# Kernel tuning notes

Hardware: AMD Instinct MI355X
Metric: run time of the kernel (lower is better)

Reference implementation:

```python
import jax, jax.numpy as jnp
import numpy as np

N_HEADS = 4

def _conv2d(x, w, b):
    # NCHW input, OIHW weight, 3x3 SAME, stride 1
    y = jax.lax.conv_general_dilated(x, w, window_strides=(1, 1), padding='SAME',
                                     dimension_numbers=('NCHW', 'OIHW', 'NCHW'))
    return y + b[None, :, None, None]


def setup_inputs() -> dict:
    key = jax.random.key(0)
    ks = jax.random.split(key, 5)
    x = jax.random.normal(ks[0], (4, 32, 256, 256), dtype=jnp.float32)
    conv1_w = jax.random.normal(ks[1], (384, 32, 3, 3), dtype=jnp.float32) * 0.05
    conv1_b = jax.random.normal(ks[2], (384,), dtype=jnp.float32) * 0.05
    conv2_w = jax.random.normal(ks[3], (32, 128, 3, 3), dtype=jnp.float32) * 0.05
    conv2_b = jax.random.normal(ks[4], (32,), dtype=jnp.float32) * 0.05
    return {'x': x, 'conv1_w': conv1_w, 'conv1_b': conv1_b,
            'conv2_w': conv2_w, 'conv2_b': conv2_b}


def reference(x, conv1_w, conv1_b, conv2_w, conv2_b):
    b, c_in, h, w = x.shape
    n = h * w
    qkv = _conv2d(x, conv1_w, conv1_b)              # [b, 3*heads*d, h, w]
    d = qkv.shape[1] // (3 * N_HEADS)               # head dim
    qkv = qkv.reshape(b, 3, N_HEADS, d, n)          # 'b (qkv heads c) h w -> b qkv heads c n'
    q, k, v = qkv[:, 0], qkv[:, 1], qkv[:, 2]
    k = jax.nn.softmax(k, axis=-1)                  # softmax over n = h*w
    weights = jnp.einsum('bhdn,bhen->bhde', q, k)   # [b, heads, d, d] context
    out = jnp.einsum('bhde,bhdn->bhen', weights, v) # [b, heads, d, n]
    out = out.reshape(b, N_HEADS * d, h, w)         # 'b heads c n -> b (heads c) h w'
    return _conv2d(out, conv2_w, conv2_b)
```

## Files before the change

kernel.cpp:

```cpp
#include <hip/hip_runtime.h>
#include <hip/hip_bf16.h>

typedef __hip_bfloat16 bf16;
typedef __attribute__((ext_vector_type(8))) short short8;
typedef __attribute__((ext_vector_type(4))) float f32x4;
typedef __attribute__((ext_vector_type(16))) float f32x16;

#define B_    4
#define CIN   32
#define HH    256
#define WW    256
#define C1    384
#define NPIX  65536
#define CMID  128
#define COUT  32
#define PW    258
#define VROW  16512

static __device__ __forceinline__ float u2f(unsigned short u) {
    unsigned int x = ((unsigned int)u) << 16;
    return __uint_as_float(x);
}
static __device__ __forceinline__ unsigned short f2u(float f) {
    bf16 h = __float2bfloat16(f);
    return __builtin_bit_cast(unsigned short, h);
}
static __device__ __forceinline__ unsigned int pk2(float lo, float hi) {
    return (unsigned int)f2u(lo) | ((unsigned int)f2u(hi) << 16);
}
static __device__ __forceinline__ void gload16(const void* src, void* dst) {
    __builtin_amdgcn_global_load_lds(
        (const __attribute__((address_space(1))) void*)src,
        (__attribute__((address_space(3))) void*)dst, 16, 0, 0);
}

__global__ __launch_bounds__(256) void k_w1t(const float* __restrict__ w1, short* __restrict__ w1t) {
    const int tap = blockIdx.x;
    for (int i = threadIdx.x; i < 384 * 32; i += 256) {
        int co = i >> 5, cij = i & 31;
        w1t[((size_t)(tap * 4 + (cij >> 3)) * 384 + co) * 8 + (cij & 7)] =
            (short)f2u(w1[(size_t)i * 9 + tap]);
    }
}

__global__ __launch_bounds__(256) void k_xt2(const float* __restrict__ x,
                                             unsigned short* __restrict__ xt2, int b0) {
    const int row = blockIdx.x, bl = blockIdx.y, b = b0 + bl;
    const int tx = threadIdx.x;
    unsigned short* rbase = xt2 + (size_t)(bl * PW + row) * 4 * PW * 8;
    const uint4 z = make_uint4(0u, 0u, 0u, 0u);
    if (row == 0 || row == PW - 1) {
        for (int i = tx; i < 4 * PW; i += 256) ((uint4*)rbase)[i] = z;
        return;
    }
    if (tx < 2) {
        int c = tx ? (PW - 1) : 0;
#pragma unroll
        for (int ch = 0; ch < 4; ch++)
            *(uint4*)(rbase + ((size_t)ch * PW + c) * 8) = z;
    }
    const int col = tx + 1;
    const size_t px = (size_t)(row - 1) * WW + tx;
    unsigned int pk[16];
#pragma unroll
    for (int c2 = 0; c2 < 16; c2++) {
        float v0 = x[((size_t)b * CIN + 2 * c2) * NPIX + px];
        float v1 = x[((size_t)b * CIN + 2 * c2 + 1) * NPIX + px];
        pk[c2] = pk2(v0, v1);
    }
#pragma unroll
    for (int ch = 0; ch < 4; ch++)
        *(uint4*)(rbase + ((size_t)ch * PW + col) * 8) =
            make_uint4(pk[ch * 4], pk[ch * 4 + 1], pk[ch * 4 + 2], pk[ch * 4 + 3]);
}

__global__ __launch_bounds__(256) void k_bordv(unsigned short* __restrict__ vt) {
    const int row = blockIdx.x, bp = blockIdx.y, tx = threadIdx.x;
    unsigned short* base = vt + ((size_t)bp * PW + row) * VROW;
    const uint4 z = make_uint4(0u, 0u, 0u, 0u);
    if (row == 0 || row == PW - 1) {
        for (int i = tx; i < VROW / 8; i += 256) ((uint4*)base)[i] = z;
    } else if (tx < 16) {
        int g = tx >> 1, c = (tx & 1) * (PW - 1);
        *(uint4*)(base + ((size_t)g * PW + c) * 8) = z;
    }
}

__global__ __launch_bounds__(256, 2) void k_conv1(
    const unsigned short* __restrict__ xt2, const short* __restrict__ w1t,
    const float* __restrict__ b1, unsigned short* __restrict__ vt,
    unsigned short* __restrict__ pw, float* __restrict__ ps, int nb)
{
    const int nblk = 512 * nb;
    const int m = ((int)blockIdx.x & 7) * (nblk >> 3) + ((int)blockIdx.x >> 3);
    const int chunk = m & 1;
    const int y   = (m >> 1) & 255;
    const int bl  = m >> 9;
    const int px0 = chunk * 128;
    const int cid = bl * 512 + y * 2 + chunk;
    const int tx  = threadIdx.x;
    const int wv  = tx >> 6, l = tx & 63;
    const int lhi = l >> 4, llo = l & 15;

    __shared__ short xs[12 * 132 * 8];
    union obuf {
        short os[64][136];
        short ost[128][66];
        short osw[4][32][32];
    };
    __shared__ obuf ou2[2];

#pragma unroll
    for (int i = 0; i < 3; i++) {
        int p = wv * 3 + i;
        int r = p >> 2, ch = p & 3;
        const char* src = (const char*)xt2 +
            (((size_t)(bl * PW) + y + r) * 4 + ch) * (PW * 16) + (size_t)px0 * 16 + (size_t)l * 16;
        char* dst = (char*)xs + p * 2112;
        gload16(src, dst);
        gload16(src + 1024, dst + 1024);
        if (l < 2) gload16(src + 2048, dst + 2048);
    }
    __syncthreads();

    const short* wbase = w1t + ((size_t)lhi * 384 + llo) * 8;

    short8 qa[2][4];
    f32x4 wacc[2][2];
#pragma unroll
    for (int dt = 0; dt < 2; dt++)
#pragma unroll
        for (int et = 0; et < 2; et++) wacc[dt][et] = (f32x4){0.f, 0.f, 0.f, 0.f};
    float se0 = 0.f, se1 = 0.f;

#pragma unroll
    for (int cog = 0; cog < 6; cog++) {
        const int co0 = cog * 64;
        const int p   = cog & 1;

        f32x4 acc[2][4];
#pragma unroll
        for (int t = 0; t < 2; t++)
#pragma unroll
            for (int mc = 0; mc < 4; mc++) acc[t][mc] = (f32x4){0.f, 0.f, 0.f, 0.f};

        short8 a[4], an[4];
#pragma unroll
        for (int mc = 0; mc < 4; mc++)
            an[mc] = *(const short8*)(wbase + ((size_t)co0 + mc * 16) * 8);
#pragma unroll
        for (int tap = 0; tap < 9; tap++) {
            const int dy = tap / 3, dx = tap % 3;
#pragma unroll
            for (int mc = 0; mc < 4; mc++) a[mc] = an[mc];
            if (tap < 8) {
#pragma unroll
                for (int mc = 0; mc < 4; mc++)
                    an[mc] = *(const short8*)(wbase +
                        ((size_t)(tap + 1) * 4 * 384 + co0 + mc * 16) * 8);
            }
#pragma unroll
            for (int t = 0; t < 2; t++) {
                short8 bfr = *(const short8*)&xs[(((dy * 4 + lhi) * 132) + (wv * 32 + t * 16 + llo + dx)) * 8];
#pragma unroll
                for (int mc = 0; mc < 4; mc++)
                    acc[t][mc] = __builtin_amdgcn_mfma_f32_16x16x32_bf16(a[mc], bfr, acc[t][mc], 0, 0, 0);
            }
        }

        float bias[4][4];
#pragma unroll
        for (int mc = 0; mc < 4; mc++)
#pragma unroll
            for (int r = 0; r < 4; r++)
                bias[mc][r] = b1[co0 + mc * 16 + lhi * 4 + r];

        if (cog < 4) {
#pragma unroll
            for (int t = 0; t < 2; t++)
#pragma unroll
                for (int mc = 0; mc < 4; mc++)
#pragma unroll
                    for (int r = 0; r < 4; r++)
                        ou2[p].os[mc * 16 + lhi * 4 + r][wv * 32 + t * 16 + llo] =
                            (short)f2u(acc[t][mc][r] + bias[mc][r]);
        } else {
#pragma unroll
            for (int t = 0; t < 2; t++)
#pragma unroll
                for (int mc = 0; mc < 4; mc++)
#pragma unroll
                    for (int r = 0; r < 4; r++)
                        ou2[p].ost[wv * 32 + t * 16 + llo][mc * 16 + lhi * 4 + r] =
                            (short)f2u(acc[t][mc][r] + bias[mc][r]);
        }
        __syncthreads();

        if (cog < 2) {
            if ((wv >> 1) == cog) {
                const int chb = (wv & 1) * 32;
#pragma unroll
                for (int dt = 0; dt < 2; dt++)
#pragma unroll
                    for (int ks = 0; ks < 4; ks++)
                        qa[dt][ks] = *(const short8*)&ou2[p].os[chb + dt * 16 + llo][ks * 32 + lhi * 8];
            }
        } else if (cog < 4) {
            if ((wv >> 1) == cog - 2) {
                const int chb = (wv & 1) * 32;
#pragma unroll
                for (int et = 0; et < 2; et++)
#pragma unroll
                    for (int ks = 0; ks < 4; ks++) {
                        short8 kf = *(const short8*)&ou2[p].os[chb + et * 16 + llo][ks * 32 + lhi * 8];
                        short8 pf;
#pragma unroll
                        for (int j = 0; j < 8; j++) {
                            float ef = __expf(u2f((unsigned short)kf[j]));
                            if (et == 0) se0 += ef; else se1 += ef;
                            pf[j] = (short)f2u(ef);
                        }
#pragma unroll
                        for (int dt = 0; dt < 2; dt++)
                            wacc[dt][et] = __builtin_amdgcn_mfma_f32_16x16x32_bf16(
                                qa[dt][ks], pf, wacc[dt][et], 0, 0, 0);
                    }
            }
        } else {
            const int plane = cog - 4;
            unsigned short* rowb = vt + ((size_t)(bl * 2 + plane) * PW + 1 + y) * VROW;
#pragma unroll
            for (int i = 0; i < 4; i++) {
                int u = i * 256 + tx;
                int g = u >> 7, px = u & 127;
                uint4 v = *(const uint4*)&ou2[p].ost[px][g * 8];
                *(uint4*)(rowb + ((size_t)g * PW + 1 + px0 + px) * 8) = v;
            }
        }
    }

    se0 += __shfl_xor(se0, 16); se0 += __shfl_xor(se0, 32);
    se1 += __shfl_xor(se1, 16); se1 += __shfl_xor(se1, 32);
    if (l < 16) {
        ps[(size_t)cid * 128 + wv * 32 + llo]      = se0;
        ps[(size_t)cid * 128 + wv * 32 + 16 + llo] = se1;
    }

#pragma unroll
    for (int dt = 0; dt < 2; dt++)
#pragma unroll
        for (int et = 0; et < 2; et++)
#pragma unroll
            for (int r = 0; r < 4; r++)
                ou2[0].osw[wv][dt * 16 + lhi * 4 + r][et * 16 + llo] = (short)f2u(wacc[dt][et][r]);
    __syncthreads();

    {
        unsigned short* pwp = pw + (size_t)cid * 4096;
        const unsigned short* osf = (const unsigned short*)&ou2[0];
#pragma unroll
        for (int p2 = 0; p2 < 2; p2++)
            *(uint4*)(pwp + p2 * 2048 + tx * 8) = *(const uint4*)(osf + p2 * 2048 + tx * 8);
    }
}

__global__ __launch_bounds__(256) void k_wred(
    const unsigned short* __restrict__ pw, const float* __restrict__ ps,
    float* __restrict__ wts, int b0)
{
    const int bh = blockIdx.x;
    const int jq = blockIdx.y;
    const int bl = bh >> 2, h = bh & 3;
    const int tx = threadIdx.x;
    __shared__ float rinvs[32];
    if (tx < 32) {
        float s = 0.f;
        const float* pp = ps + (size_t)bl * 512 * 128 + h * 32 + tx;
        for (int c = 0; c < 512; c++) s += pp[(size_t)c * 128];
        rinvs[tx] = 1.f / s;
    }
    __syncthreads();
    const int i = jq * 256 + tx;
    const unsigned short* pwp = pw + (size_t)bl * 512 * 4096 + h * 1024 + i;
    float s = 0.f;
    for (int c = 0; c < 512; c++) s += u2f(pwp[(size_t)c * 4096]);
    wts[(size_t)(b0 * 4 + bh) * 1024 + i] = s * rinvs[i & 31];
}

__global__ __launch_bounds__(256) void k_w2e(
    const float* __restrict__ w2, const float* __restrict__ wts,
    short* __restrict__ w2te, int b0)
{
    const int bl = blockIdx.x, tap = blockIdx.y;
    const int tx = threadIdx.x;
    __shared__ float Wsh[4096];
    __shared__ float w2sh[4096];
    for (int i = tx; i < 4096; i += 256) {
        Wsh[i]  = wts[(size_t)(b0 + bl) * 4096 + i];
        w2sh[i] = w2[(size_t)i * 9 + tap];
    }
    __syncthreads();
#pragma unroll
    for (int rep = 0; rep < 16; rep++) {
        int o = rep * 256 + tx;
        int cv = o >> 5, co = o & 31;
        int h = cv >> 5, d = cv & 31;
        const float* wp = &w2sh[co * 128 + 32 * h];
        const float* Wp = &Wsh[h * 1024 + d * 32];
        float s = 0.f;
#pragma unroll
        for (int e = 0; e < 32; e++) s += wp[e] * Wp[e];
        w2te[((((size_t)bl * 9 + tap) * 16 + (cv >> 3)) * 32 + co) * 8 + (cv & 7)] =
            (short)f2u(s);
    }
}

__global__ __launch_bounds__(256, 2) void k_conv2e(
    const unsigned short* __restrict__ vt, const short* __restrict__ w2te,
    const float* __restrict__ b2, float* __restrict__ out, int b0, int nb)
{
    const int nblk = 512 * nb;
    const int m = ((int)blockIdx.x & 7) * (nblk >> 3) + ((int)blockIdx.x >> 3);
    const int chunk = m & 1;
    const int y   = (m >> 1) & 255;
    const int bl  = m >> 9;
    const int px0 = chunk * 128;
    const int bb  = b0 + bl;
    const int tx  = threadIdx.x;
    const int wv  = tx >> 6, l = tx & 63;
    const int lhi = l >> 4, llo = l & 15;

    __shared__ short xs2[2][12 * 132 * 8];
    __shared__ float osf[32][132];

    const short* w2b = w2te + (size_t)bl * 9 * 16 * 32 * 8;

    float bias[2][4];
#pragma unroll
    for (int mm = 0; mm < 2; mm++)
#pragma unroll
        for (int r = 0; r < 4; r++)
            bias[mm][r] = b2[mm * 16 + lhi * 4 + r];

    f32x4 acc[2][2];
#pragma unroll
    for (int t = 0; t < 2; t++)
#pragma unroll
        for (int mm = 0; mm < 2; mm++) acc[t][mm] = (f32x4){0.f, 0.f, 0.f, 0.f};

#pragma unroll
    for (int i = 0; i < 3; i++) {
        int p = wv * 3 + i;
        int r = p >> 2, sg = p & 3;
        const char* src = (const char*)vt +
            (((size_t)(bl * 2 + 0) * PW + y + r) * VROW
             + ((size_t)(0 * 4 + sg) * PW + px0) * 8) * 2 + (size_t)l * 16;
        char* dst = (char*)xs2[0] + p * 2112;
        gload16(src, dst);
        gload16(src + 1024, dst + 1024);
        if (l < 2) gload16(src + 2048, dst + 2048);
    }

#pragma unroll
    for (int cc = 0; cc < 4; cc++) {
        __syncthreads();

        if (cc < 3) {
            const int nplane = (cc + 1) >> 1, nghalf = (cc + 1) & 1;
#pragma unroll
            for (int i = 0; i < 3; i++) {
                int p = wv * 3 + i;
                int r = p >> 2, sg = p & 3;
                const char* src = (const char*)vt +
                    (((size_t)(bl * 2 + nplane) * PW + y + r) * VROW
                     + ((size_t)(nghalf * 4 + sg) * PW + px0) * 8) * 2 + (size_t)l * 16;
                char* dst = (char*)xs2[(cc + 1) & 1] + p * 2112;
                gload16(src, dst);
                gload16(src + 1024, dst + 1024);
                if (l < 2) gload16(src + 2048, dst + 2048);
            }
        }

        const short* xsc = xs2[cc & 1];
        short8 a[2], an[2];
#pragma unroll
        for (int mm = 0; mm < 2; mm++)
            an[mm] = *(const short8*)(w2b + ((size_t)(cc * 4 + lhi) * 32 + mm * 16 + llo) * 8);
#pragma unroll
        for (int tap = 0; tap < 9; tap++) {
            const int dy = tap / 3, dx = tap % 3;
#pragma unroll
            for (int mm = 0; mm < 2; mm++) a[mm] = an[mm];
            if (tap < 8) {
#pragma unroll
                for (int mm = 0; mm < 2; mm++)
                    an[mm] = *(const short8*)(w2b +
                        ((size_t)((tap + 1) * 16 + cc * 4 + lhi) * 32 + mm * 16 + llo) * 8);
            }
#pragma unroll
            for (int t = 0; t < 2; t++) {
                short8 bfr = *(const short8*)&xsc[(((dy * 4 + lhi) * 132) + (wv * 32 + t * 16 + llo + dx)) * 8];
#pragma unroll
                for (int mm = 0; mm < 2; mm++)
                    acc[t][mm] = __builtin_amdgcn_mfma_f32_16x16x32_bf16(a[mm], bfr, acc[t][mm], 0, 0, 0);
            }
        }
    }

    __syncthreads();
#pragma unroll
    for (int t = 0; t < 2; t++)
#pragma unroll
        for (int mm = 0; mm < 2; mm++)
#pragma unroll
            for (int r = 0; r < 4; r++)
                osf[mm * 16 + lhi * 4 + r][wv * 32 + t * 16 + llo] = acc[t][mm][r] + bias[mm][r];
    __syncthreads();
#pragma unroll
    for (int p = 0; p < 4; p++) {
        int chl = p * 8 + (tx >> 5);
        float4 v = *(const float4*)&osf[chl][(tx & 31) * 4];
        *(float4*)(out + ((size_t)bb * COUT + chl) * NPIX + y * WW + px0 + (tx & 31) * 4) = v;
    }
}

extern "C" void kernel_launch(void* const* d_in, const int* in_sizes, int n_in,
                              void* d_out, int out_size, void* d_ws, size_t ws_size,
                              hipStream_t stream) {
    const float* x  = (const float*)d_in[0];
    const float* w1 = (const float*)d_in[1];
    const float* b1 = (const float*)d_in[2];
    const float* w2 = (const float*)d_in[3];
    const float* b2 = (const float*)d_in[4];
    float* out = (float*)d_out;

    char* ws = (char*)d_ws;
    float* wts  = (float*)(ws + 4096);
    short* w1t  = (short*)(ws + 69632);
    short* w2te = (short*)(ws + 364544);
    const size_t OFF_XT = 1048576;

    int nb = 4;
    size_t xt_sz = (size_t)nb * PW * 4 * PW * 16;
    size_t pw_sz = (size_t)nb * 512 * 4096 * 2;
    size_t ps_sz = (size_t)nb * 512 * 128 * 4;
    size_t vt_sz = (size_t)nb * 2 * PW * (size_t)VROW * 2;
    if (ws_size < OFF_XT + xt_sz + pw_sz + ps_sz + vt_sz) {
        nb = 1;
        xt_sz = (size_t)nb * PW * 4 * PW * 16;
        pw_sz = (size_t)nb * 512 * 4096 * 2;
        ps_sz = (size_t)nb * 512 * 128 * 4;
        vt_sz = (size_t)nb * 2 * PW * (size_t)VROW * 2;
    }
    const size_t pw_off = OFF_XT + xt_sz;
    const size_t ps_off = pw_off + pw_sz;
    const size_t vt_off = ps_off + ps_sz;

    unsigned short* xt2 = (unsigned short*)(ws + OFF_XT);
    unsigned short* pw  = (unsigned short*)(ws + pw_off);
    float*          psb = (float*)(ws + ps_off);
    unsigned short* vt  = (unsigned short*)(ws + vt_off);

    k_w1t<<<dim3(9), 256, 0, stream>>>(w1, w1t);

    for (int b0 = 0; b0 < B_; b0 += nb) {
        k_xt2  <<<dim3(PW, nb),      256, 0, stream>>>(x, xt2, b0);
        k_bordv<<<dim3(PW, nb * 2),  256, 0, stream>>>(vt);
        k_conv1<<<dim3(2 * HH * nb), 256, 0, stream>>>(xt2, w1t, b1, vt, pw, psb, nb);
        k_wred <<<dim3(nb * 4, 4),   256, 0, stream>>>(pw, psb, wts, b0);
        k_w2e  <<<dim3(nb, 9),       256, 0, stream>>>(w2, wts, w2te, b0);
        k_conv2e<<<dim3(2 * HH * nb),256, 0, stream>>>(vt, w2te, b2, out, b0, nb);
    }
}
```

Measured before the change: 186.7 us.

## Process a full image row per conv1 block instead of half-row chunks

Each k_conv1 block now computes all 256 pixels of a row, with each wave handling 64 pixels, instead of one of two 128-pixel chunks. The point is to reuse every loaded weight fragment across twice as many MFMAs, halve the number of blocks and partial results, and shrink the k_wred reduction. The output staging buffer is no longer double-buffered and gets written in two halves with extra barriers. The accumulator registers double, which risks lower occupancy under launch_bounds(256,2) and fewer blocks to fill the GPU.

```diff
diff --git a/kernel.cpp b/kernel.cpp
--- a/kernel.cpp
+++ b/kernel.cpp
@@ -91,41 +91,40 @@
     const float* __restrict__ b1, unsigned short* __restrict__ vt,
     unsigned short* __restrict__ pw, float* __restrict__ ps, int nb)
 {
-    const int nblk = 512 * nb;
+    const int nblk = 256 * nb;
     const int m = ((int)blockIdx.x & 7) * (nblk >> 3) + ((int)blockIdx.x >> 3);
-    const int chunk = m & 1;
-    const int y   = (m >> 1) & 255;
-    const int bl  = m >> 9;
-    const int px0 = chunk * 128;
-    const int cid = bl * 512 + y * 2 + chunk;
+    const int y   = m & 255;
+    const int bl  = m >> 8;
+    const int cid = bl * 256 + y;
     const int tx  = threadIdx.x;
     const int wv  = tx >> 6, l = tx & 63;
     const int lhi = l >> 4, llo = l & 15;
 
-    __shared__ short xs[12 * 132 * 8];
-    union obuf {
+    __shared__ short xs[12 * 258 * 8];
+    __shared__ union {
         short os[64][136];
         short ost[128][66];
         short osw[4][32][32];
-    };
-    __shared__ obuf ou2[2];
+    } ou;
 
 #pragma unroll
     for (int i = 0; i < 3; i++) {
         int p = wv * 3 + i;
         int r = p >> 2, ch = p & 3;
         const char* src = (const char*)xt2 +
-            (((size_t)(bl * PW) + y + r) * 4 + ch) * (PW * 16) + (size_t)px0 * 16 + (size_t)l * 16;
-        char* dst = (char*)xs + p * 2112;
+            (((size_t)(bl * PW) + y + r) * 4 + ch) * (PW * 16) + (size_t)l * 16;
+        char* dst = (char*)xs + p * 4128;
         gload16(src, dst);
         gload16(src + 1024, dst + 1024);
-        if (l < 2) gload16(src + 2048, dst + 2048);
+        gload16(src + 2048, dst + 2048);
+        gload16(src + 3072, dst + 3072);
+        if (l < 2) gload16(src + 4096, dst + 4096);
     }
     __syncthreads();
 
     const short* wbase = w1t + ((size_t)lhi * 384 + llo) * 8;
 
-    short8 qa[2][4];
+    short8 qa[2][8];
     f32x4 wacc[2][2];
 #pragma unroll
     for (int dt = 0; dt < 2; dt++)
@@ -136,11 +135,10 @@
 #pragma unroll
     for (int cog = 0; cog < 6; cog++) {
         const int co0 = cog * 64;
-        const int p   = cog & 1;
-
-        f32x4 acc[2][4];
-#pragma unroll
-        for (int t = 0; t < 2; t++)
+
+        f32x4 acc[4][4];
+#pragma unroll
+        for (int t = 0; t < 4; t++)
 #pragma unroll
             for (int mc = 0; mc < 4; mc++) acc[t][mc] = (f32x4){0.f, 0.f, 0.f, 0.f};
 
@@ -160,8 +158,8 @@
                         ((size_t)(tap + 1) * 4 * 384 + co0 + mc * 16) * 8);
             }
 #pragma unroll
-            for (int t = 0; t < 2; t++) {
-                short8 bfr = *(const short8*)&xs[(((dy * 4 + lhi) * 132) + (wv * 32 + t * 16 + llo + dx)) * 8];
+            for (int t = 0; t < 4; t++) {
+                short8 bfr = *(const short8*)&xs[(((dy * 4 + lhi) * 258) + (wv * 64 + t * 16 + llo + dx)) * 8];
 #pragma unroll
                 for (int mc = 0; mc < 4; mc++)
                     acc[t][mc] = __builtin_amdgcn_mfma_f32_16x16x32_bf16(a[mc], bfr, acc[t][mc], 0, 0, 0);
@@ -175,66 +173,74 @@
             for (int r = 0; r < 4; r++)
                 bias[mc][r] = b1[co0 + mc * 16 + lhi * 4 + r];
 
-        if (cog < 4) {
-#pragma unroll
-            for (int t = 0; t < 2; t++)
-#pragma unroll
-                for (int mc = 0; mc < 4; mc++)
-#pragma unroll
-                    for (int r = 0; r < 4; r++)
-                        ou2[p].os[mc * 16 + lhi * 4 + r][wv * 32 + t * 16 + llo] =
-                            (short)f2u(acc[t][mc][r] + bias[mc][r]);
-        } else {
-#pragma unroll
-            for (int t = 0; t < 2; t++)
-#pragma unroll
-                for (int mc = 0; mc < 4; mc++)
-#pragma unroll
-                    for (int r = 0; r < 4; r++)
-                        ou2[p].ost[wv * 32 + t * 16 + llo][mc * 16 + lhi * 4 + r] =
-                            (short)f2u(acc[t][mc][r] + bias[mc][r]);
-        }
-        __syncthreads();
-
-        if (cog < 2) {
-            if ((wv >> 1) == cog) {
-                const int chb = (wv & 1) * 32;
-#pragma unroll
-                for (int dt = 0; dt < 2; dt++)
-#pragma unroll
-                    for (int ks = 0; ks < 4; ks++)
-                        qa[dt][ks] = *(const short8*)&ou2[p].os[chb + dt * 16 + llo][ks * 32 + lhi * 8];
-            }
-        } else if (cog < 4) {
-            if ((wv >> 1) == cog - 2) {
-                const int chb = (wv & 1) * 32;
-#pragma unroll
-                for (int et = 0; et < 2; et++)
-#pragma unroll
-                    for (int ks = 0; ks < 4; ks++) {
-                        short8 kf = *(const short8*)&ou2[p].os[chb + et * 16 + llo][ks * 32 + lhi * 8];
-                        short8 pf;
-#pragma unroll
-                        for (int j = 0; j < 8; j++) {
-                            float ef = __expf(u2f((unsigned short)kf[j]));
-                            if (et == 0) se0 += ef; else se1 += ef;
-                            pf[j] = (short)f2u(ef);
+#pragma unroll
+        for (int h2 = 0; h2 < 2; h2++) {
+            __syncthreads();
+            if ((wv >> 1) == h2) {
+                const int pxl0 = (wv & 1) * 64;
+                if (cog < 4) {
+#pragma unroll
+                    for (int t = 0; t < 4; t++)
+#pragma unroll
+                        for (int mc = 0; mc < 4; mc++)
+#pragma unroll
+                            for (int r = 0; r < 4; r++)
+                                ou.os[mc * 16 + lhi * 4 + r][pxl0 + t * 16 + llo] =
+                                    (short)f2u(acc[t][mc][r] + bias[mc][r]);
+                } else {
+#pragma unroll
+                    for (int t = 0; t < 4; t++)
+#pragma unroll
+                        for (int mc = 0; mc < 4; mc++)
+#pragma unroll
+                            for (int r = 0; r < 4; r++)
+                                ou.ost[pxl0 + t * 16 + llo][mc * 16 + lhi * 4 + r] =
+                                    (short)f2u(acc[t][mc][r] + bias[mc][r]);
+                }
+            }
+            __syncthreads();
+
+            if (cog < 2) {
+                if ((wv >> 1) == cog) {
+                    const int chb = (wv & 1) * 32;
+#pragma unroll
+                    for (int dt = 0; dt < 2; dt++)
+#pragma unroll
+                        for (int ks = 0; ks < 4; ks++)
+                            qa[dt][h2 * 4 + ks] =
+                                *(const short8*)&ou.os[chb + dt * 16 + llo][ks * 32 + lhi * 8];
+                }
+            } else if (cog < 4) {
+                if ((wv >> 1) == cog - 2) {
+                    const int chb = (wv & 1) * 32;
+#pragma unroll
+                    for (int et = 0; et < 2; et++)
+#pragma unroll
+                        for (int ks = 0; ks < 4; ks++) {
+                            short8 kf = *(const short8*)&ou.os[chb + et * 16 + llo][ks * 32 + lhi * 8];
+                            short8 pf;
+#pragma unroll
+                            for (int j = 0; j < 8; j++) {
+                                float ef = __expf(u2f((unsigned short)kf[j]));
+                                if (et == 0) se0 += ef; else se1 += ef;
+                                pf[j] = (short)f2u(ef);
+                            }
+#pragma unroll
+                            for (int dt = 0; dt < 2; dt++)
+                                wacc[dt][et] = __builtin_amdgcn_mfma_f32_16x16x32_bf16(
+                                    qa[dt][h2 * 4 + ks], pf, wacc[dt][et], 0, 0, 0);
                         }
-#pragma unroll
-                        for (int dt = 0; dt < 2; dt++)
-                            wacc[dt][et] = __builtin_amdgcn_mfma_f32_16x16x32_bf16(
-                                qa[dt][ks], pf, wacc[dt][et], 0, 0, 0);
-                    }
-            }
-        } else {
-            const int plane = cog - 4;
-            unsigned short* rowb = vt + ((size_t)(bl * 2 + plane) * PW + 1 + y) * VROW;
-#pragma unroll
-            for (int i = 0; i < 4; i++) {
-                int u = i * 256 + tx;
-                int g = u >> 7, px = u & 127;
-                uint4 v = *(const uint4*)&ou2[p].ost[px][g * 8];
-                *(uint4*)(rowb + ((size_t)g * PW + 1 + px0 + px) * 8) = v;
+                }
+            } else {
+                const int plane = cog - 4;
+                unsigned short* rowb = vt + ((size_t)(bl * 2 + plane) * PW + 1 + y) * VROW;
+#pragma unroll
+                for (int i = 0; i < 4; i++) {
+                    int u = i * 256 + tx;
+                    int g = u >> 7, px = u & 127;
+                    uint4 v = *(const uint4*)&ou.ost[px][g * 8];
+                    *(uint4*)(rowb + ((size_t)g * PW + 1 + h2 * 128 + px) * 8) = v;
+                }
             }
         }
     }
@@ -246,18 +252,19 @@
         ps[(size_t)cid * 128 + wv * 32 + 16 + llo] = se1;
     }
 
+    __syncthreads();
 #pragma unroll
     for (int dt = 0; dt < 2; dt++)
 #pragma unroll
         for (int et = 0; et < 2; et++)
 #pragma unroll
             for (int r = 0; r < 4; r++)
-                ou2[0].osw[wv][dt * 16 + lhi * 4 + r][et * 16 + llo] = (short)f2u(wacc[dt][et][r]);
+                ou.osw[wv][dt * 16 + lhi * 4 + r][et * 16 + llo] = (short)f2u(wacc[dt][et][r]);
     __syncthreads();
 
     {
         unsigned short* pwp = pw + (size_t)cid * 4096;
-        const unsigned short* osf = (const unsigned short*)&ou2[0];
+        const unsigned short* osf = (const unsigned short*)&ou;
 #pragma unroll
         for (int p2 = 0; p2 < 2; p2++)
             *(uint4*)(pwp + p2 * 2048 + tx * 8) = *(const uint4*)(osf + p2 * 2048 + tx * 8);
@@ -275,15 +282,15 @@
     __shared__ float rinvs[32];
     if (tx < 32) {
         float s = 0.f;
-        const float* pp = ps + (size_t)bl * 512 * 128 + h * 32 + tx;
-        for (int c = 0; c < 512; c++) s += pp[(size_t)c * 128];
+        const float* pp = ps + (size_t)bl * 256 * 128 + h * 32 + tx;
+        for (int c = 0; c < 256; c++) s += pp[(size_t)c * 128];
         rinvs[tx] = 1.f / s;
     }
     __syncthreads();
     const int i = jq * 256 + tx;
-    const unsigned short* pwp = pw + (size_t)bl * 512 * 4096 + h * 1024 + i;
+    const unsigned short* pwp = pw + (size_t)bl * 256 * 4096 + h * 1024 + i;
     float s = 0.f;
-    for (int c = 0; c < 512; c++) s += u2f(pwp[(size_t)c * 4096]);
+    for (int c = 0; c < 256; c++) s += u2f(pwp[(size_t)c * 4096]);
     wts[(size_t)(b0 * 4 + bh) * 1024 + i] = s * rinvs[i & 31];
 }
 
@@ -442,14 +449,14 @@
 
     int nb = 4;
     size_t xt_sz = (size_t)nb * PW * 4 * PW * 16;
-    size_t pw_sz = (size_t)nb * 512 * 4096 * 2;
-    size_t ps_sz = (size_t)nb * 512 * 128 * 4;
+    size_t pw_sz = (size_t)nb * 256 * 4096 * 2;
+    size_t ps_sz = (size_t)nb * 256 * 128 * 4;
     size_t vt_sz = (size_t)nb * 2 * PW * (size_t)VROW * 2;
     if (ws_size < OFF_XT + xt_sz + pw_sz + ps_sz + vt_sz) {
         nb = 1;
         xt_sz = (size_t)nb * PW * 4 * PW * 16;
-        pw_sz = (size_t)nb * 512 * 4096 * 2;
-        ps_sz = (size_t)nb * 512 * 128 * 4;
+        pw_sz = (size_t)nb * 256 * 4096 * 2;
+        ps_sz = (size_t)nb * 256 * 128 * 4;
         vt_sz = (size_t)nb * 2 * PW * (size_t)VROW * 2;
     }
     const size_t pw_off = OFF_XT + xt_sz;
@@ -466,7 +473,7 @@
     for (int b0 = 0; b0 < B_; b0 += nb) {
         k_xt2  <<<dim3(PW, nb),      256, 0, stream>>>(x, xt2, b0);
         k_bordv<<<dim3(PW, nb * 2),  256, 0, stream>>>(vt);
-        k_conv1<<<dim3(2 * HH * nb), 256, 0, stream>>>(xt2, w1t, b1, vt, pw, psb, nb);
+        k_conv1<<<dim3(HH * nb),     256, 0, stream>>>(xt2, w1t, b1, vt, pw, psb, nb);
         k_wred <<<dim3(nb * 4, 4),   256, 0, stream>>>(pw, psb, wts, b0);
         k_w2e  <<<dim3(nb, 9),       256, 0, stream>>>(w2, wts, w2te, b0);
         k_conv2e<<<dim3(2 * HH * nb),256, 0, stream>>>(vt, w2te, b2, out, b0, nb);
```

Result: no change. 184.1 us (-1.4%).

## Stage conv1 weights in LDS via async loads and single-buffer output tile

Applied to the files above, without the earlier changes.

Conv1 weights for each 64-channel group are now loaded cooperatively into shared memory with async global-to-LDS loads, instead of each lane fetching its MFMA A-fragments straight from global memory. The next group's weights are prefetched while the current output tile is written. The double-buffered output staging union becomes a single buffer, with an extra barrier per group to make reuse safe. This aims to cut redundant global and L2 weight traffic, but it adds block-wide synchronisation and removes the overlap the double buffer provided.

```diff
diff --git a/kernel.cpp b/kernel.cpp
--- a/kernel.cpp
+++ b/kernel.cpp
@@ -103,12 +103,12 @@
     const int lhi = l >> 4, llo = l & 15;
 
     __shared__ short xs[12 * 132 * 8];
-    union obuf {
+    __shared__ short wt[9][4][64][8];
+    __shared__ union {
         short os[64][136];
         short ost[128][66];
         short osw[4][32][32];
-    };
-    __shared__ obuf ou2[2];
+    } ou;
 
 #pragma unroll
     for (int i = 0; i < 3; i++) {
@@ -121,9 +121,14 @@
         gload16(src + 1024, dst + 1024);
         if (l < 2) gload16(src + 2048, dst + 2048);
     }
-    __syncthreads();
-
-    const short* wbase = w1t + ((size_t)lhi * 384 + llo) * 8;
+#pragma unroll
+    for (int i = 0; i < 9; i++) {
+        int s = wv * 9 + i;
+        int tap = s >> 2, ch = s & 3;
+        const char* src = (const char*)w1t + ((size_t)(tap * 4 + ch) * 384) * 16 + (size_t)l * 16;
+        gload16(src, (char*)&wt[tap][ch][0][0]);
+    }
+    __syncthreads();
 
     short8 qa[2][4];
     f32x4 wacc[2][2];
@@ -136,7 +141,6 @@
 #pragma unroll
     for (int cog = 0; cog < 6; cog++) {
         const int co0 = cog * 64;
-        const int p   = cog & 1;
 
         f32x4 acc[2][4];
 #pragma unroll
@@ -144,21 +148,13 @@
 #pragma unroll
             for (int mc = 0; mc < 4; mc++) acc[t][mc] = (f32x4){0.f, 0.f, 0.f, 0.f};
 
-        short8 a[4], an[4];
-#pragma unroll
-        for (int mc = 0; mc < 4; mc++)
-            an[mc] = *(const short8*)(wbase + ((size_t)co0 + mc * 16) * 8);
 #pragma unroll
         for (int tap = 0; tap < 9; tap++) {
             const int dy = tap / 3, dx = tap % 3;
-#pragma unroll
-            for (int mc = 0; mc < 4; mc++) a[mc] = an[mc];
-            if (tap < 8) {
-#pragma unroll
-                for (int mc = 0; mc < 4; mc++)
-                    an[mc] = *(const short8*)(wbase +
-                        ((size_t)(tap + 1) * 4 * 384 + co0 + mc * 16) * 8);
-            }
+            short8 a[4];
+#pragma unroll
+            for (int mc = 0; mc < 4; mc++)
+                a[mc] = *(const short8*)&wt[tap][lhi][mc * 16 + llo][0];
 #pragma unroll
             for (int t = 0; t < 2; t++) {
                 short8 bfr = *(const short8*)&xs[(((dy * 4 + lhi) * 132) + (wv * 32 + t * 16 + llo + dx)) * 8];
@@ -175,6 +171,8 @@
             for (int r = 0; r < 4; r++)
                 bias[mc][r] = b1[co0 + mc * 16 + lhi * 4 + r];
 
+        __syncthreads();
+
         if (cog < 4) {
 #pragma unroll
             for (int t = 0; t < 2; t++)
@@ -182,7 +180,7 @@
                 for (int mc = 0; mc < 4; mc++)
 #pragma unroll
                     for (int r = 0; r < 4; r++)
-                        ou2[p].os[mc * 16 + lhi * 4 + r][wv * 32 + t * 16 + llo] =
+                        ou.os[mc * 16 + lhi * 4 + r][wv * 32 + t * 16 + llo] =
                             (short)f2u(acc[t][mc][r] + bias[mc][r]);
         } else {
 #pragma unroll
@@ -191,8 +189,19 @@
                 for (int mc = 0; mc < 4; mc++)
 #pragma unroll
                     for (int r = 0; r < 4; r++)
-                        ou2[p].ost[wv * 32 + t * 16 + llo][mc * 16 + lhi * 4 + r] =
+                        ou.ost[wv * 32 + t * 16 + llo][mc * 16 + lhi * 4 + r] =
                             (short)f2u(acc[t][mc][r] + bias[mc][r]);
+        }
+
+        if (cog < 5) {
+#pragma unroll
+            for (int i = 0; i < 9; i++) {
+                int s = wv * 9 + i;
+                int tap = s >> 2, ch = s & 3;
+                const char* src = (const char*)w1t +
+                    ((size_t)(tap * 4 + ch) * 384 + co0 + 64) * 16 + (size_t)l * 16;
+                gload16(src, (char*)&wt[tap][ch][0][0]);
+            }
         }
         __syncthreads();
 
@@ -203,7 +212,7 @@
                 for (int dt = 0; dt < 2; dt++)
 #pragma unroll
                     for (int ks = 0; ks < 4; ks++)
-                        qa[dt][ks] = *(const short8*)&ou2[p].os[chb + dt * 16 + llo][ks * 32 + lhi * 8];
+                        qa[dt][ks] = *(const short8*)&ou.os[chb + dt * 16 + llo][ks * 32 + lhi * 8];
             }
         } else if (cog < 4) {
             if ((wv >> 1) == cog - 2) {
@@ -212,7 +221,7 @@
                 for (int et = 0; et < 2; et++)
 #pragma unroll
                     for (int ks = 0; ks < 4; ks++) {
-                        short8 kf = *(const short8*)&ou2[p].os[chb + et * 16 + llo][ks * 32 + lhi * 8];
+                        short8 kf = *(const short8*)&ou.os[chb + et * 16 + llo][ks * 32 + lhi * 8];
                         short8 pf;
 #pragma unroll
                         for (int j = 0; j < 8; j++) {
@@ -233,7 +242,7 @@
             for (int i = 0; i < 4; i++) {
                 int u = i * 256 + tx;
                 int g = u >> 7, px = u & 127;
-                uint4 v = *(const uint4*)&ou2[p].ost[px][g * 8];
+                uint4 v = *(const uint4*)&ou.ost[px][g * 8];
                 *(uint4*)(rowb + ((size_t)g * PW + 1 + px0 + px) * 8) = v;
             }
         }
@@ -246,18 +255,19 @@
         ps[(size_t)cid * 128 + wv * 32 + 16 + llo] = se1;
     }
 
+    __syncthreads();
 #pragma unroll
     for (int dt = 0; dt < 2; dt++)
 #pragma unroll
         for (int et = 0; et < 2; et++)
 #pragma unroll
             for (int r = 0; r < 4; r++)
-                ou2[0].osw[wv][dt * 16 + lhi * 4 + r][et * 16 + llo] = (short)f2u(wacc[dt][et][r]);
+                ou.osw[wv][dt * 16 + lhi * 4 + r][et * 16 + llo] = (short)f2u(wacc[dt][et][r]);
     __syncthreads();
 
     {
         unsigned short* pwp = pw + (size_t)cid * 4096;
-        const unsigned short* osf = (const unsigned short*)&ou2[0];
+        const unsigned short* osf = (const unsigned short*)&ou;
 #pragma unroll
         for (int p2 = 0; p2 < 2; p2++)
             *(uint4*)(pwp + p2 * 2048 + tx * 8) = *(const uint4*)(osf + p2 * 2048 + tx * 8);
```

Result: slower. 196.6 us (+5.3%).
